# Performance work log

Hardware: AMD Instinct MI355X
Metric: run time of the kernel (lower is better)

The kernel has to match this reference:

```python
import jax, jax.numpy as jnp
import numpy as np


def setup_inputs() -> dict:
    key = jax.random.key(0)
    k1, k2, k3, k4, k5 = jax.random.split(key, 5)
    B, N, T, O, G = 32, 256, 1024, 1024, 8
    x = jax.random.normal(k1, (B, N, T), dtype=jnp.float32)
    y = jax.random.uniform(k2, (B, G), dtype=jnp.float32)  # genre mixture weights
    weight = jax.random.normal(k3, (G, O, T), dtype=jnp.float32) * (1.0 / np.sqrt(T))
    mask = jax.random.uniform(k4, (O, T), dtype=jnp.float32)
    bias = jax.random.normal(k5, (O,), dtype=jnp.float32)
    return {"x": x, "y": y, "weight": weight, "mask": mask, "bias": bias}


def reference(x, y, weight, mask, bias):
    # mask the shared weight bank: [G,O,T] * [1,O,T]
    masked_w = weight * mask[None, :, :]
    # per-sample genre-mixed weights: [B,G] x [G,O,T] -> [B,O,T]
    w_bot = jnp.einsum('bg,got->bot', y, masked_w)
    # batched masked linear: [B,N,T] x [B,O,T] -> [B,N,O], plus bias
    return jnp.einsum('bnt,bot->bno', x, w_bot) + bias
```

## Files before the change

kernel.cpp:

```cpp
#include <hip/hip_runtime.h>
#include <hip/hip_bf16.h>
#include <stdint.h>


#define B_ 32
#define N_ 256
#define T_ 1024
#define O_ 1024
#define G_ 8

#define WSTRIDE ((size_t)(O_ * T_ + 2048))

#define BM 128
#define BN 128
#define BK 64
#define BUFSZ (BM * BK)

typedef __attribute__((__ext_vector_type__(8)))  __bf16 bf16x8;
typedef __attribute__((__ext_vector_type__(16))) float  f32x16;

__device__ __forceinline__ unsigned short f2bf(float f) {
    union { float f; uint32_t u; } v; v.f = f;
    uint32_t u = v.u;
    uint32_t r = (u + 0x7fffu + ((u >> 16) & 1u)) >> 16;
    return (unsigned short)r;
}

__device__ __forceinline__ uint4 pack8(const float* a) {
    uint4 r;
    r.x = (uint32_t)f2bf(a[0]) | ((uint32_t)f2bf(a[1]) << 16);
    r.y = (uint32_t)f2bf(a[2]) | ((uint32_t)f2bf(a[3]) << 16);
    r.z = (uint32_t)f2bf(a[4]) | ((uint32_t)f2bf(a[5]) << 16);
    r.w = (uint32_t)f2bf(a[6]) | ((uint32_t)f2bf(a[7]) << 16);
    return r;
}

#define MIXB 1024
#define CVTB 1024

__global__ __launch_bounds__(256) void prep_kernel(
    const float* __restrict__ w,
    const float* __restrict__ mask,
    const float* __restrict__ y,
    const float* __restrict__ x,
    unsigned short* __restrict__ Wb,
    unsigned short* __restrict__ xb)
{
    const int tid = threadIdx.x;
    if (blockIdx.x < MIXB) {
        const int bhalf = blockIdx.x & 1;
        const int grp   = blockIdx.x >> 1;
        const int idx   = grp * 256 + tid;
        const int o     = idx >> 7;
        const int t     = (idx & 127) << 3;

        const float* mrow = mask + (size_t)o * T_ + t;
        const float4 m0 = *(const float4*)(mrow);
        const float4 m1 = *(const float4*)(mrow + 4);

        float wv[G_][8];
#pragma unroll
        for (int g = 0; g < G_; ++g) {
            const float* wrow = w + ((size_t)g * O_ + o) * T_ + t;
            const float4 a0 = *(const float4*)(wrow);
            const float4 a1 = *(const float4*)(wrow + 4);
            wv[g][0] = a0.x * m0.x; wv[g][1] = a0.y * m0.y;
            wv[g][2] = a0.z * m0.z; wv[g][3] = a0.w * m0.w;
            wv[g][4] = a1.x * m1.x; wv[g][5] = a1.y * m1.y;
            wv[g][6] = a1.z * m1.z; wv[g][7] = a1.w * m1.w;
        }
        unsigned short* dst = Wb + (size_t)o * T_ + t;
        const int bph = grp & 15;
#pragma unroll 4
        for (int bi = 0; bi < 16; ++bi) {
            const int b = bhalf * 16 + ((bi + bph) & 15);
            const float4 y0 = *(const float4*)(y + b * G_);
            const float4 y1 = *(const float4*)(y + b * G_ + 4);
            const float yv[G_] = {y0.x, y0.y, y0.z, y0.w, y1.x, y1.y, y1.z, y1.w};
            float acc[8] = {};
#pragma unroll
            for (int g = 0; g < G_; ++g)
#pragma unroll
                for (int j = 0; j < 8; ++j)
                    acc[j] += yv[g] * wv[g][j];
            *(uint4*)(dst + (size_t)b * WSTRIDE) = pack8(acc);
        }
    } else {
        const int i = (blockIdx.x - MIXB) * 256 + tid;
        const float4* x4 = (const float4*)x;
        uint4* o4 = (uint4*)xb;
#pragma unroll
        for (int j = 0; j < 4; ++j) {
            const size_t f4 = (size_t)j * 524288 + (size_t)i * 2;
            const float4 a = x4[f4];
            const float4 b = x4[f4 + 1];
            const float v[8] = {a.x, a.y, a.z, a.w, b.x, b.y, b.z, b.w};
            o4[(size_t)j * 262144 + i] = pack8(v);
        }
    }
}

__device__ __forceinline__ void load16_to_lds(const unsigned short* g, unsigned short* l) {
    __builtin_amdgcn_global_load_lds(
        (const __attribute__((address_space(1))) unsigned char*)g,
        (__attribute__((address_space(3))) unsigned char*)l,
        16, 0, 0);
}

__global__ __launch_bounds__(256, 2) void gemm_kernel(
    const unsigned short* __restrict__ xb,
    const unsigned short* __restrict__ Wb,
    const float* __restrict__ bias,
    float* __restrict__ out)
{
    __shared__ __align__(16) unsigned short lA[2 * BUFSZ];
    __shared__ __align__(16) unsigned short lB[2 * BUFSZ];

    const int tn = blockIdx.x;
    const int tm = blockIdx.y;
    const int b  = blockIdx.z;

    const int tid  = threadIdx.x;
    const int lane = tid & 63;
    const int wave = tid >> 6;
    const int wm   = (wave >> 1) * 64;
    const int wn   = (wave & 1) * 64;

    const unsigned short* Ab = xb + (size_t)b * N_ * T_ + (size_t)(tm * BM) * T_;
    const unsigned short* Bb = Wb + (size_t)b * WSTRIDE + (size_t)(tn * BN) * T_;

    const int srow   = tid >> 3;
    const int schunk = (tid & 7) ^ (srow & 7);
    const unsigned short* ga0 = Ab + (size_t)srow * T_ + schunk * 8;
    const unsigned short* gb0 = Bb + (size_t)srow * T_ + schunk * 8;

#define STAGE(buf, kt)                                                          \
    {                                                                           \
        unsigned short* lad = lA + (buf) * BUFSZ + tid * 8;                     \
        unsigned short* lbd = lB + (buf) * BUFSZ + tid * 8;                     \
        _Pragma("unroll")                                                       \
        for (int i_ = 0; i_ < 4; ++i_) {                                        \
            load16_to_lds(ga0 + (kt) + (size_t)(i_ * 32) * T_, lad + i_ * 2048);\
            load16_to_lds(gb0 + (kt) + (size_t)(i_ * 32) * T_, lbd + i_ * 2048);\
        }                                                                       \
    }

    f32x16 acc[2][2] = {};

    const int fr   = lane & 31;
    const int half = lane >> 5;
    const int sw   = fr & 7;

#define COMPUTE(buf)                                                            \
    {                                                                           \
        const unsigned short* la = lA + (buf) * BUFSZ;                          \
        const unsigned short* lb = lB + (buf) * BUFSZ;                          \
        _Pragma("unroll")                                                       \
        for (int ks = 0; ks < 4; ++ks) {                                        \
            const int cp = (((ks * 2 + half)) ^ sw) * 8;                        \
            bf16x8 afr[2], bfr[2];                                              \
            _Pragma("unroll")                                                   \
            for (int i_ = 0; i_ < 2; ++i_)                                      \
                afr[i_] = *(const bf16x8*)(la + (wm + i_ * 32 + fr) * BK + cp); \
            _Pragma("unroll")                                                   \
            for (int i_ = 0; i_ < 2; ++i_)                                      \
                bfr[i_] = *(const bf16x8*)(lb + (wn + i_ * 32 + fr) * BK + cp); \
            _Pragma("unroll")                                                   \
            for (int mi = 0; mi < 2; ++mi)                                      \
                _Pragma("unroll")                                               \
                for (int ni = 0; ni < 2; ++ni)                                  \
                    acc[mi][ni] = __builtin_amdgcn_mfma_f32_32x32x16_bf16(      \
                        afr[mi], bfr[ni], acc[mi][ni], 0, 0, 0);                \
        }                                                                       \
    }

    STAGE(0, 0)
    for (int kt = 0; kt < T_; kt += 2 * BK) {
        __syncthreads();
        STAGE(1, kt + BK)
        COMPUTE(0)
        __syncthreads();
        if (kt + 2 * BK < T_) STAGE(0, kt + 2 * BK)
        COMPUTE(1)
    }

    float* outb = out + (size_t)b * N_ * O_ + (size_t)(tm * BM) * O_ + (tn * BN);
    const int cn = lane & 31;
    const int rb = (lane >> 5) * 4;
#pragma unroll
    for (int ni = 0; ni < 2; ++ni) {
        const int col = wn + ni * 32 + cn;
        const float bv = bias[tn * BN + col];
#pragma unroll
        for (int mi = 0; mi < 2; ++mi) {
#pragma unroll
            for (int r = 0; r < 16; ++r) {
                const int row = wm + mi * 32 + rb + (r & 3) + 8 * (r >> 2);
                outb[(size_t)row * O_ + col] = acc[mi][ni][r] + bv;
            }
        }
    }
}

__global__ __launch_bounds__(256) void naive_kernel(
    const float* __restrict__ x, const float* __restrict__ y,
    const float* __restrict__ w, const float* __restrict__ mask,
    const float* __restrict__ bias, float* __restrict__ out)
{
    const int oc = blockIdx.x & 3;
    const int n  = (blockIdx.x >> 2) & (N_ - 1);
    const int b  = blockIdx.x >> 10;

    __shared__ float xs[T_];
    __shared__ float ys[G_];
    const float* xrow = x + ((size_t)b * N_ + n) * T_;
    for (int i = threadIdx.x; i < T_ / 4; i += 256)
        ((float4*)xs)[i] = ((const float4*)xrow)[i];
    if (threadIdx.x < G_) ys[threadIdx.x] = y[b * G_ + threadIdx.x];
    __syncthreads();

    const int o = oc * 256 + threadIdx.x;
    float acc = 0.f;
    for (int t = 0; t < T_; t += 4) {
        const float4 m4 = *(const float4*)(mask + (size_t)o * T_ + t);
        float4 s = {0.f, 0.f, 0.f, 0.f};
#pragma unroll
        for (int g = 0; g < G_; ++g) {
            const float4 w4 = *(const float4*)(w + ((size_t)g * O_ + o) * T_ + t);
            const float yv = ys[g];
            s.x += yv * w4.x; s.y += yv * w4.y; s.z += yv * w4.z; s.w += yv * w4.w;
        }
        acc += xs[t] * m4.x * s.x + xs[t + 1] * m4.y * s.y
             + xs[t + 2] * m4.z * s.z + xs[t + 3] * m4.w * s.w;
    }
    out[((size_t)b * N_ + n) * O_ + o] = acc + bias[o];
}

extern "C" void kernel_launch(void* const* d_in, const int* in_sizes, int n_in,
                              void* d_out, int out_size, void* d_ws, size_t ws_size,
                              hipStream_t stream) {
    const float* x    = (const float*)d_in[0];
    const float* y    = (const float*)d_in[1];
    const float* w    = (const float*)d_in[2];
    const float* mask = (const float*)d_in[3];
    const float* bias = (const float*)d_in[4];
    float* out = (float*)d_out;

    const size_t wb_bytes = (size_t)B_ * WSTRIDE * sizeof(unsigned short);
    const size_t xb_bytes = (size_t)B_ * N_ * T_ * sizeof(unsigned short);

    if (ws_size >= wb_bytes + xb_bytes) {
        unsigned short* Wb = (unsigned short*)d_ws;
        unsigned short* xb = (unsigned short*)((char*)d_ws + wb_bytes);
        prep_kernel<<<MIXB + CVTB, 256, 0, stream>>>(w, mask, y, x, Wb, xb);
        dim3 grid(O_ / BN, N_ / BM, B_);
        gemm_kernel<<<grid, 256, 0, stream>>>(xb, Wb, bias, out);
    } else {
        naive_kernel<<<B_ * N_ * (O_ / 256), 256, 0, stream>>>(x, y, w, mask, bias, out);
    }
}
```

Baseline: 167.2 us.

## Store mixed weights as [O,B,T] and mix all batches per prep thread

Mixed bf16 weights change layout from [B,O,T] with a padded per-batch stride to [O,B,T], so each prep thread writes all 32 batches of a row contiguously. The prep mix stage uses half as many blocks, each covering every batch and reading y from shared memory, which halves the re-reading of weight and mask. The GEMM B-tile loads now stride by B*T between rows, which changes DRAM and L2 access locality for the GEMM and removes the padding that was meant to avoid channel conflicts.

```diff
diff --git a/kernel.cpp b/kernel.cpp
--- a/kernel.cpp
+++ b/kernel.cpp
@@ -9,12 +9,12 @@
 #define O_ 1024
 #define G_ 8
 
-#define WSTRIDE ((size_t)(O_ * T_ + 2048))
-
 #define BM 128
 #define BN 128
 #define BK 64
 #define BUFSZ (BM * BK)
+
+#define BROW ((size_t)(B_ * T_))
 
 typedef __attribute__((__ext_vector_type__(8)))  __bf16 bf16x8;
 typedef __attribute__((__ext_vector_type__(16))) float  f32x16;
@@ -35,7 +35,7 @@
     return r;
 }
 
-#define MIXB 1024
+#define MIXB 512
 #define CVTB 1024
 
 __global__ __launch_bounds__(256) void prep_kernel(
@@ -48,11 +48,13 @@
 {
     const int tid = threadIdx.x;
     if (blockIdx.x < MIXB) {
-        const int bhalf = blockIdx.x & 1;
-        const int grp   = blockIdx.x >> 1;
-        const int idx   = grp * 256 + tid;
-        const int o     = idx >> 7;
-        const int t     = (idx & 127) << 3;
+        __shared__ float ys[B_ * G_];
+        ys[tid] = y[tid];
+        __syncthreads();
+
+        const int idx = blockIdx.x * 256 + tid;
+        const int o   = idx >> 7;
+        const int t   = (idx & 127) << 3;
 
         const float* mrow = mask + (size_t)o * T_ + t;
         const float4 m0 = *(const float4*)(mrow);
@@ -69,13 +71,13 @@
             wv[g][4] = a1.x * m1.x; wv[g][5] = a1.y * m1.y;
             wv[g][6] = a1.z * m1.z; wv[g][7] = a1.w * m1.w;
         }
-        unsigned short* dst = Wb + (size_t)o * T_ + t;
-        const int bph = grp & 15;
+        unsigned short* dst = Wb + (size_t)o * BROW + t;
+        const int bph = blockIdx.x & (B_ - 1);
 #pragma unroll 4
-        for (int bi = 0; bi < 16; ++bi) {
-            const int b = bhalf * 16 + ((bi + bph) & 15);
-            const float4 y0 = *(const float4*)(y + b * G_);
-            const float4 y1 = *(const float4*)(y + b * G_ + 4);
+        for (int bi = 0; bi < B_; ++bi) {
+            const int b = (bi + bph) & (B_ - 1);
+            const float4 y0 = *(const float4*)(ys + b * G_);
+            const float4 y1 = *(const float4*)(ys + b * G_ + 4);
             const float yv[G_] = {y0.x, y0.y, y0.z, y0.w, y1.x, y1.y, y1.z, y1.w};
             float acc[8] = {};
 #pragma unroll
@@ -83,7 +85,7 @@
 #pragma unroll
                 for (int j = 0; j < 8; ++j)
                     acc[j] += yv[g] * wv[g][j];
-            *(uint4*)(dst + (size_t)b * WSTRIDE) = pack8(acc);
+            *(uint4*)(dst + (size_t)b * T_) = pack8(acc);
         }
     } else {
         const int i = (blockIdx.x - MIXB) * 256 + tid;
@@ -127,12 +129,12 @@
     const int wn   = (wave & 1) * 64;
 
     const unsigned short* Ab = xb + (size_t)b * N_ * T_ + (size_t)(tm * BM) * T_;
-    const unsigned short* Bb = Wb + (size_t)b * WSTRIDE + (size_t)(tn * BN) * T_;
+    const unsigned short* Bb = Wb + (size_t)(tn * BN) * BROW + (size_t)b * T_;
 
     const int srow   = tid >> 3;
     const int schunk = (tid & 7) ^ (srow & 7);
     const unsigned short* ga0 = Ab + (size_t)srow * T_ + schunk * 8;
-    const unsigned short* gb0 = Bb + (size_t)srow * T_ + schunk * 8;
+    const unsigned short* gb0 = Bb + (size_t)srow * BROW + schunk * 8;
 
 #define STAGE(buf, kt)                                                          \
     {                                                                           \
@@ -141,7 +143,7 @@
         _Pragma("unroll")                                                       \
         for (int i_ = 0; i_ < 4; ++i_) {                                        \
             load16_to_lds(ga0 + (kt) + (size_t)(i_ * 32) * T_, lad + i_ * 2048);\
-            load16_to_lds(gb0 + (kt) + (size_t)(i_ * 32) * T_, lbd + i_ * 2048);\
+            load16_to_lds(gb0 + (kt) + (size_t)(i_ * 32) * BROW, lbd + i_ * 2048);\
         }                                                                       \
     }
 
@@ -246,7 +248,7 @@
     const float* bias = (const float*)d_in[4];
     float* out = (float*)d_out;
 
-    const size_t wb_bytes = (size_t)B_ * WSTRIDE * sizeof(unsigned short);
+    const size_t wb_bytes = (size_t)O_ * B_ * T_ * sizeof(unsigned short);
     const size_t xb_bytes = (size_t)B_ * N_ * T_ * sizeof(unsigned short);
 
     if (ws_size >= wb_bytes + xb_bytes) {
```

Measured after the change: 156.5 us. -6.4%, faster.
